# Performance work log

Hardware: AMD Instinct MI355X
Metric: run time of the kernel (lower is better)

Reference implementation:

```python
import jax, jax.numpy as jnp
import numpy as np

N, M, C = 2048, 32, 1024  # persons, max_others, dim_inner


def setup_inputs() -> dict:
    key = jax.random.key(0)
    k1, k2, k3, k4, k5, k6 = jax.random.split(key, 6)
    return {
        "person_features": jax.random.normal(k1, (N, C, 1, 1), dtype=jnp.float32),
        "other_features": jax.random.normal(k2, (N, M, C, 1, 1), dtype=jnp.float32),
        "person_boxes": jax.random.uniform(k3, (N, 4), dtype=jnp.float32),
        "other_boxes": jax.random.uniform(k4, (N, M, 4), dtype=jnp.float32),
        "is_person": jnp.ones((N, M), dtype=bool),
        "W": jax.random.normal(k5, (C, 2 * C), dtype=jnp.float32) / np.sqrt(2 * C),
        "b": jax.random.normal(k6, (C,), dtype=jnp.float32) * 0.01,
    }


def reference(person_features, other_features, person_boxes, other_boxes, is_person, W, b):
    # person_features: [n, c, 1, 1]; other_features: [n, m, c, 1, 1]
    p = person_features[:, :, 0, 0]        # [n, c]
    o = other_features[:, :, :, 0, 0]      # [n, m, c]
    # Linear on concat([p, o]) == p @ Wp^T + o @ Wo^T + b with W = [Wp | Wo]
    Wp, Wo = W[:, :p.shape[1]], W[:, p.shape[1]:]
    pk = jnp.einsum('nc,dc->nd', p, Wp)            # shared across others
    ok = jnp.einsum('nmc,dc->nmd', o, Wo)
    x = pk[:, None, :] + ok + b                    # [n, m, d]
    x = jnp.max(x, axis=1)                         # max-pool over others
    return x[:, :, None, None]                     # [n, d, 1, 1]
```

## Files before the change

### kernel.cpp

```cpp
#include <hip/hip_runtime.h>
#include <hip/hip_bf16.h>


#define NN 2048
#define MM 32
#define CC 1024

typedef __attribute__((ext_vector_type(8))) __bf16 bf16x8;
typedef __attribute__((ext_vector_type(4))) float f32x4;
typedef __attribute__((ext_vector_type(8))) unsigned short u16x8;
typedef __attribute__((ext_vector_type(4))) unsigned short u16x4;

__device__ inline unsigned short f2bf(float f) {
  union { __hip_bfloat16 h; unsigned short u; } v;
  v.h = __float2bfloat16(f);
  return v.u;
}

__device__ inline void gload_lds16(const void* g, void* l) {
  __builtin_amdgcn_global_load_lds(
      (const __attribute__((address_space(1))) void*)g,
      (__attribute__((address_space(3))) void*)l, 16, 0, 0);
}

__global__ void conv_pw(const float* __restrict__ p, const float* __restrict__ W,
                        unsigned short* __restrict__ pd,
                        unsigned short* __restrict__ wp,
                        unsigned short* __restrict__ wo) {
  const int PG = (NN * CC) / 8;
  const int WG = (CC * 2 * CC) / 8;
  int i = blockIdx.x * blockDim.x + threadIdx.x;
  int stride = gridDim.x * blockDim.x;
  for (; i < PG + WG; i += stride) {
    if (i < PG) {
      const float4* s = reinterpret_cast<const float4*>(p) + (size_t)i * 2;
      float4 a = s[0], b = s[1];
      u16x8 r;
      r[0] = f2bf(a.x); r[1] = f2bf(a.y); r[2] = f2bf(a.z); r[3] = f2bf(a.w);
      r[4] = f2bf(b.x); r[5] = f2bf(b.y); r[6] = f2bf(b.z); r[7] = f2bf(b.w);
      *reinterpret_cast<u16x8*>(pd + (size_t)i * 8) = r;
    } else {
      int f = i - PG;
      int e = f * 8;
      int d = e >> 11;
      int cc = e & 2047;
      const float4* s = reinterpret_cast<const float4*>(W) + (size_t)f * 2;
      float4 a = s[0], b = s[1];
      u16x8 r;
      r[0] = f2bf(a.x); r[1] = f2bf(a.y); r[2] = f2bf(a.z); r[3] = f2bf(a.w);
      r[4] = f2bf(b.x); r[5] = f2bf(b.y); r[6] = f2bf(b.z); r[7] = f2bf(b.w);
      unsigned short* o = (cc < CC) ? (wp + (size_t)d * CC + cc)
                                    : (wo + (size_t)d * CC + (cc - CC));
      *reinterpret_cast<u16x8*>(o) = r;
    }
  }
}

__global__ void gemm_pk(const unsigned short* __restrict__ A,
                        const unsigned short* __restrict__ B,
                        const float* __restrict__ bvec,
                        float* __restrict__ out) {
  __shared__ unsigned short As[128 * 64];
  __shared__ unsigned short Bs[128 * 64];

  int nb = gridDim.x;
  int chunk = nb >> 3;
  int obid = blockIdx.x;
  int vb = (obid & 7) * chunk + (obid >> 3);
  int bcol = vb & 7;
  int brow = vb >> 3;

  int tid = threadIdx.x;
  int l = tid & 63;
  int wid = tid >> 6;
  int wr = wid >> 1, wc = wid & 1;
  int lr = l & 15;
  int lk = (l >> 4) << 3;

  const unsigned short* gA = A + (size_t)brow * 128 * CC;
  const unsigned short* gB = B + (size_t)bcol * 128 * CC;

  f32x4 acc[4][4] = {};

  for (int kt = 0; kt < 16; ++kt) {
    int k0 = kt * 64;
#pragma unroll
    for (int j = 0; j < 4; ++j) {
      int f = (j * 256 + tid) * 8;
      int r = f >> 6;
      int c = f & 63;
      gload_lds16(gA + (size_t)r * CC + k0 + c, &As[f]);
      gload_lds16(gB + (size_t)r * CC + k0 + c, &Bs[f]);
    }
    __syncthreads();
#pragma unroll
    for (int kk = 0; kk < 2; ++kk) {
      bf16x8 af[4], bfr[4];
#pragma unroll
      for (int mi = 0; mi < 4; ++mi)
        af[mi] = *reinterpret_cast<const bf16x8*>(
            &As[(wr * 64 + mi * 16 + lr) * 64 + kk * 32 + lk]);
#pragma unroll
      for (int ni = 0; ni < 4; ++ni)
        bfr[ni] = *reinterpret_cast<const bf16x8*>(
            &Bs[(wc * 64 + ni * 16 + lr) * 64 + kk * 32 + lk]);
#pragma unroll
      for (int mi = 0; mi < 4; ++mi)
#pragma unroll
        for (int ni = 0; ni < 4; ++ni)
          acc[mi][ni] = __builtin_amdgcn_mfma_f32_16x16x32_bf16(
              af[mi], bfr[ni], acc[mi][ni], 0, 0, 0);
    }
    __syncthreads();
  }

#pragma unroll
  for (int mi = 0; mi < 4; ++mi) {
    int row = brow * 128 + wr * 64 + mi * 16 + (l >> 4) * 4;
#pragma unroll
    for (int ni = 0; ni < 4; ++ni) {
      int col = bcol * 128 + wc * 64 + ni * 16 + lr;
      float bb = bvec[col];
#pragma unroll
      for (int r = 0; r < 4; ++r)
        out[(size_t)(row + r) * CC + col] = acc[mi][ni][r] + bb;
    }
  }
}


#define BARRIER                                      \
  do {                                               \
    asm volatile("" ::: "memory");                   \
    __builtin_amdgcn_s_barrier();                    \
    asm volatile("" ::: "memory");                   \
  } while (0)

#define LGKM0 asm volatile("s_waitcnt lgkmcnt(0)" ::: "memory")
#define VMCNT(n) asm volatile("s_waitcnt vmcnt(" #n ")" ::: "memory")

#define STAGE_B(k0)                                                           \
  do {                                                                        \
    _Pragma("unroll") for (int j = 0; j < 4; ++j)                             \
        gload_lds16(gB + (size_t)(j * 64 + brr) * CC + (k0) + bsc,            \
                    lds + 16384 + ((j * 512 + tid) * 16));                    \
  } while (0)

#define ISSUE_A(k0)                                                           \
  do {                                                                        \
    _Pragma("unroll") for (int j = 0; j < 4; ++j)                             \
        aL[j] = *reinterpret_cast<const float4*>(                             \
            gAf + (size_t)(j * 32 + arow0) * CC + (k0) + ac4 * 4);            \
  } while (0)

#define CVT_WRITE_A                                                           \
  do {                                                                        \
    _Pragma("unroll") for (int j = 0; j < 4; ++j) {                           \
      u16x4 r;                                                                \
      r[0] = f2bf(aL[j].x); r[1] = f2bf(aL[j].y);                             \
      r[2] = f2bf(aL[j].z); r[3] = f2bf(aL[j].w);                             \
      *reinterpret_cast<u16x4*>(lds + (j * 32 + arow0) * 128 + aswz) = r;     \
    }                                                                         \
  } while (0)

#define MFMA16X                                                               \
  do {                                                                        \
    __builtin_amdgcn_s_setprio(1);                                            \
    _Pragma("unroll") for (int mi = 0; mi < 4; ++mi)                          \
        _Pragma("unroll") for (int ni = 0; ni < 4; ++ni)                      \
            acc[mi][ni] = __builtin_amdgcn_mfma_f32_16x16x32_bf16(            \
                af[mi], bfr[ni], acc[mi][ni], 0, 0, 0);                       \
    __builtin_amdgcn_s_setprio(0);                                            \
  } while (0)

__global__ __launch_bounds__(512, 4) void gemm_fused(
    const float* __restrict__ A,
    const unsigned short* __restrict__ B,
    const float* __restrict__ pkb,
    float* __restrict__ out) {
  __shared__ char lds[49152];

  int obid = blockIdx.x;
  int vb = (obid & 7) * 256 + (obid >> 3);
  int bcol = vb & 3;
  int brow = vb >> 2;

  int tid = threadIdx.x;
  int l = tid & 63;
  int wid = tid >> 6;
  int wr = wid >> 2;
  int wc = wid & 3;
  int lr = l & 15;
  int g = l >> 4;

  const float* gAf = A + (size_t)brow * 128 * CC;
  const unsigned short* gB = B + (size_t)bcol * 256 * CC;

  int brr = tid >> 3;
  int bsc = ((tid & 7) ^ ((tid >> 3) & 7)) * 8;

  int arow0 = tid >> 4;
  int ac4 = tid & 15;
  int aswz = (((ac4 >> 1) ^ (arow0 & 7)) * 16) + (ac4 & 1) * 8;

  int axor = lr & 7;
  int a_k0 = (wr * 64 + lr) * 128 + ((g ^ axor) * 16);
  int a_k1 = (wr * 64 + lr) * 128 + (((4 + g) ^ axor) * 16);
  int b_k0 = 16384 + (wc * 64 + lr) * 128 + ((g ^ axor) * 16);
  int b_k1 = 16384 + (wc * 64 + lr) * 128 + (((4 + g) ^ axor) * 16);

  f32x4 acc[4][4] = {};
  bf16x8 af[4], bfr[4];
  float4 aL[4];

  ISSUE_A(0);

#pragma unroll 1
  for (int t = 0; t < 16; ++t) {
    BARRIER;
    VMCNT(0);
    CVT_WRITE_A;
    STAGE_B(t * 64);
    if (t + 1 < 16) ISSUE_A((t + 1) * 64);
    LGKM0;
    if (t + 1 < 16) { VMCNT(4); } else { VMCNT(0); }
    BARRIER;
#pragma unroll
    for (int mi = 0; mi < 4; ++mi)
      af[mi] = *(const bf16x8*)(lds + a_k0 + mi * 2048);
#pragma unroll
    for (int ni = 0; ni < 4; ++ni)
      bfr[ni] = *(const bf16x8*)(lds + b_k0 + ni * 2048);
    LGKM0;
    MFMA16X;
#pragma unroll
    for (int mi = 0; mi < 4; ++mi)
      af[mi] = *(const bf16x8*)(lds + a_k1 + mi * 2048);
#pragma unroll
    for (int ni = 0; ni < 4; ++ni)
      bfr[ni] = *(const bf16x8*)(lds + b_k1 + ni * 2048);
    LGKM0;
    MFMA16X;
  }

#pragma unroll
  for (int a = 0; a < 2; ++a) {
    int n = brow * 4 + wr * 2 + a;
#pragma unroll
    for (int ni = 0; ni < 4; ++ni) {
      float v = -3.402823466e38f;
#pragma unroll
      for (int mi = 2 * a; mi < 2 * a + 2; ++mi)
#pragma unroll
        for (int r = 0; r < 4; ++r) v = fmaxf(v, acc[mi][ni][r]);
      v = fmaxf(v, __shfl_xor(v, 16));
      v = fmaxf(v, __shfl_xor(v, 32));
      if (l < 16) {
        int col = bcol * 256 + wc * 64 + ni * 16 + l;
        out[(size_t)n * CC + col] = v + pkb[(size_t)n * CC + col];
      }
    }
  }
}

extern "C" void kernel_launch(void* const* d_in, const int* in_sizes, int n_in,
                              void* d_out, int out_size, void* d_ws, size_t ws_size,
                              hipStream_t stream) {
  const float* p = (const float*)d_in[0];
  const float* o = (const float*)d_in[1];
  const float* W = (const float*)d_in[5];
  const float* b = (const float*)d_in[6];
  float* out = (float*)d_out;

  char* ws = (char*)d_ws;
  unsigned short* p_bf  = (unsigned short*)ws;
  unsigned short* wp_bf = (unsigned short*)(ws + 4194304);
  unsigned short* wo_bf = (unsigned short*)(ws + 6291456);
  float*          pkb   = (float*)(ws + 8388608);

  conv_pw<<<512, 256, 0, stream>>>(p, W, p_bf, wp_bf, wo_bf);
  gemm_pk<<<128, 256, 0, stream>>>(p_bf, wp_bf, b, pkb);
  gemm_fused<<<2048, 512, 0, stream>>>(o, wo_bf, pkb, out);
}
```

Before: 178.6 us.

## Fuse bf16 conversion and person GEMM into a single prep kernel

Folds the standalone fp32→bf16 conversion kernel and the person-feature GEMM into one launch. Blocks 0-511 convert only the Wo half of W, and the remaining 128 blocks run the pk GEMM straight from fp32 p and Wp. Those blocks convert in registers, write to swizzled LDS, and prefetch the next K-tile into registers. This removes one launch plus the bf16 round trip through memory for p and Wp. In exchange, the GEMM blocks read twice as many bytes as fp32 and do the conversion work inline.

```diff
diff --git a/kernel.cpp b/kernel.cpp
--- a/kernel.cpp
+++ b/kernel.cpp
@@ -23,50 +23,39 @@
       (__attribute__((address_space(3))) void*)l, 16, 0, 0);
 }
 
-__global__ void conv_pw(const float* __restrict__ p, const float* __restrict__ W,
-                        unsigned short* __restrict__ pd,
-                        unsigned short* __restrict__ wp,
-                        unsigned short* __restrict__ wo) {
-  const int PG = (NN * CC) / 8;
-  const int WG = (CC * 2 * CC) / 8;
-  int i = blockIdx.x * blockDim.x + threadIdx.x;
-  int stride = gridDim.x * blockDim.x;
-  for (; i < PG + WG; i += stride) {
-    if (i < PG) {
-      const float4* s = reinterpret_cast<const float4*>(p) + (size_t)i * 2;
-      float4 a = s[0], b = s[1];
-      u16x8 r;
-      r[0] = f2bf(a.x); r[1] = f2bf(a.y); r[2] = f2bf(a.z); r[3] = f2bf(a.w);
-      r[4] = f2bf(b.x); r[5] = f2bf(b.y); r[6] = f2bf(b.z); r[7] = f2bf(b.w);
-      *reinterpret_cast<u16x8*>(pd + (size_t)i * 8) = r;
-    } else {
-      int f = i - PG;
-      int e = f * 8;
-      int d = e >> 11;
-      int cc = e & 2047;
-      const float4* s = reinterpret_cast<const float4*>(W) + (size_t)f * 2;
-      float4 a = s[0], b = s[1];
-      u16x8 r;
-      r[0] = f2bf(a.x); r[1] = f2bf(a.y); r[2] = f2bf(a.z); r[3] = f2bf(a.w);
-      r[4] = f2bf(b.x); r[5] = f2bf(b.y); r[6] = f2bf(b.z); r[7] = f2bf(b.w);
-      unsigned short* o = (cc < CC) ? (wp + (size_t)d * CC + cc)
-                                    : (wo + (size_t)d * CC + (cc - CC));
-      *reinterpret_cast<u16x8*>(o) = r;
-    }
-  }
-}
-
-__global__ void gemm_pk(const unsigned short* __restrict__ A,
-                        const unsigned short* __restrict__ B,
-                        const float* __restrict__ bvec,
-                        float* __restrict__ out) {
-  __shared__ unsigned short As[128 * 64];
-  __shared__ unsigned short Bs[128 * 64];
-
-  int nb = gridDim.x;
-  int chunk = nb >> 3;
-  int obid = blockIdx.x;
-  int vb = (obid & 7) * chunk + (obid >> 3);
+#define BARRIER                                      \
+  do {                                               \
+    asm volatile("" ::: "memory");                   \
+    __builtin_amdgcn_s_barrier();                    \
+    asm volatile("" ::: "memory");                   \
+  } while (0)
+
+#define LGKM0 asm volatile("s_waitcnt lgkmcnt(0)" ::: "memory")
+#define VMCNT(n) asm volatile("s_waitcnt vmcnt(" #n ")" ::: "memory")
+
+__global__ __launch_bounds__(256, 2) void prep(
+    const float* __restrict__ p,
+    const float* __restrict__ W,
+    const float* __restrict__ bvec,
+    unsigned short* __restrict__ wo,
+    float* __restrict__ pkb) {
+  if (blockIdx.x < 512) {
+    int i = blockIdx.x * 256 + threadIdx.x;
+    int e = i * 8;
+    int d = e >> 10;
+    int c = e & 1023;
+    const float4* s = reinterpret_cast<const float4*>(W + (size_t)d * 2048 + CC + c);
+    float4 a = s[0], b = s[1];
+    u16x8 r;
+    r[0] = f2bf(a.x); r[1] = f2bf(a.y); r[2] = f2bf(a.z); r[3] = f2bf(a.w);
+    r[4] = f2bf(b.x); r[5] = f2bf(b.y); r[6] = f2bf(b.z); r[7] = f2bf(b.w);
+    *reinterpret_cast<u16x8*>(wo + (size_t)d * CC + c) = r;
+    return;
+  }
+
+  __shared__ char lds[32768];
+  int obid = blockIdx.x - 512;
+  int vb = (obid & 7) * 16 + (obid >> 3);
   int bcol = vb & 7;
   int brow = vb >> 3;
 
@@ -75,43 +64,82 @@
   int wid = tid >> 6;
   int wr = wid >> 1, wc = wid & 1;
   int lr = l & 15;
-  int lk = (l >> 4) << 3;
-
-  const unsigned short* gA = A + (size_t)brow * 128 * CC;
-  const unsigned short* gB = B + (size_t)bcol * 128 * CC;
+  int g = l >> 4;
+
+  const float* gP = p + (size_t)brow * 128 * CC;
+  const float* gW = W + (size_t)bcol * 128 * 2048;
+
+  int arow0 = tid >> 4;
+  int ac4 = tid & 15;
+  int aswz = (((ac4 >> 1) ^ (arow0 & 7)) * 16) + (ac4 & 1) * 8;
+
+  int axor = lr & 7;
+  int a_k0 = (wr * 64 + lr) * 128 + ((g ^ axor) * 16);
+  int a_k1 = (wr * 64 + lr) * 128 + (((4 + g) ^ axor) * 16);
+  int b_k0 = 16384 + (wc * 64 + lr) * 128 + ((g ^ axor) * 16);
+  int b_k1 = 16384 + (wc * 64 + lr) * 128 + (((4 + g) ^ axor) * 16);
 
   f32x4 acc[4][4] = {};
-
-  for (int kt = 0; kt < 16; ++kt) {
-    int k0 = kt * 64;
-#pragma unroll
-    for (int j = 0; j < 4; ++j) {
-      int f = (j * 256 + tid) * 8;
-      int r = f >> 6;
-      int c = f & 63;
-      gload_lds16(gA + (size_t)r * CC + k0 + c, &As[f]);
-      gload_lds16(gB + (size_t)r * CC + k0 + c, &Bs[f]);
-    }
-    __syncthreads();
-#pragma unroll
-    for (int kk = 0; kk < 2; ++kk) {
-      bf16x8 af[4], bfr[4];
-#pragma unroll
-      for (int mi = 0; mi < 4; ++mi)
-        af[mi] = *reinterpret_cast<const bf16x8*>(
-            &As[(wr * 64 + mi * 16 + lr) * 64 + kk * 32 + lk]);
-#pragma unroll
-      for (int ni = 0; ni < 4; ++ni)
-        bfr[ni] = *reinterpret_cast<const bf16x8*>(
-            &Bs[(wc * 64 + ni * 16 + lr) * 64 + kk * 32 + lk]);
-#pragma unroll
-      for (int mi = 0; mi < 4; ++mi)
-#pragma unroll
-        for (int ni = 0; ni < 4; ++ni)
-          acc[mi][ni] = __builtin_amdgcn_mfma_f32_16x16x32_bf16(
-              af[mi], bfr[ni], acc[mi][ni], 0, 0, 0);
-    }
-    __syncthreads();
+  bf16x8 af[4], bfr[4];
+  float4 aL[8], bL[8];
+
+#define ISSUE_P(k0)                                                           \
+  do {                                                                        \
+    _Pragma("unroll") for (int j = 0; j < 8; ++j)                             \
+        aL[j] = *reinterpret_cast<const float4*>(                             \
+            gP + (size_t)(j * 16 + arow0) * CC + (k0) + ac4 * 4);             \
+  } while (0)
+#define ISSUE_W(k0)                                                           \
+  do {                                                                        \
+    _Pragma("unroll") for (int j = 0; j < 8; ++j)                             \
+        bL[j] = *reinterpret_cast<const float4*>(                             \
+            gW + (size_t)(j * 16 + arow0) * 2048 + (k0) + ac4 * 4);           \
+  } while (0)
+#define CVT_WR(src, base)                                                     \
+  do {                                                                        \
+    _Pragma("unroll") for (int j = 0; j < 8; ++j) {                           \
+      u16x4 r;                                                                \
+      r[0] = f2bf(src[j].x); r[1] = f2bf(src[j].y);                           \
+      r[2] = f2bf(src[j].z); r[3] = f2bf(src[j].w);                           \
+      *reinterpret_cast<u16x4*>(lds + (base) + (j * 16 + arow0) * 128 + aswz) = r; \
+    }                                                                         \
+  } while (0)
+#define PK_MFMA                                                               \
+  do {                                                                        \
+    _Pragma("unroll") for (int mi = 0; mi < 4; ++mi)                          \
+        _Pragma("unroll") for (int ni = 0; ni < 4; ++ni)                      \
+            acc[mi][ni] = __builtin_amdgcn_mfma_f32_16x16x32_bf16(            \
+                af[mi], bfr[ni], acc[mi][ni], 0, 0, 0);                       \
+  } while (0)
+
+  ISSUE_P(0);
+  ISSUE_W(0);
+
+#pragma unroll 1
+  for (int t = 0; t < 16; ++t) {
+    BARRIER;
+    VMCNT(0);
+    CVT_WR(aL, 0);
+    CVT_WR(bL, 16384);
+    if (t + 1 < 16) { ISSUE_P((t + 1) * 64); ISSUE_W((t + 1) * 64); }
+    LGKM0;
+    BARRIER;
+#pragma unroll
+    for (int mi = 0; mi < 4; ++mi)
+      af[mi] = *(const bf16x8*)(lds + a_k0 + mi * 2048);
+#pragma unroll
+    for (int ni = 0; ni < 4; ++ni)
+      bfr[ni] = *(const bf16x8*)(lds + b_k0 + ni * 2048);
+    LGKM0;
+    PK_MFMA;
+#pragma unroll
+    for (int mi = 0; mi < 4; ++mi)
+      af[mi] = *(const bf16x8*)(lds + a_k1 + mi * 2048);
+#pragma unroll
+    for (int ni = 0; ni < 4; ++ni)
+      bfr[ni] = *(const bf16x8*)(lds + b_k1 + ni * 2048);
+    LGKM0;
+    PK_MFMA;
   }
 
 #pragma unroll
@@ -123,21 +151,15 @@
       float bb = bvec[col];
 #pragma unroll
       for (int r = 0; r < 4; ++r)
-        out[(size_t)(row + r) * CC + col] = acc[mi][ni][r] + bb;
+        pkb[(size_t)(row + r) * CC + col] = acc[mi][ni][r] + bb;
     }
   }
-}
-
-
-#define BARRIER                                      \
-  do {                                               \
-    asm volatile("" ::: "memory");                   \
-    __builtin_amdgcn_s_barrier();                    \
-    asm volatile("" ::: "memory");                   \
-  } while (0)
-
-#define LGKM0 asm volatile("s_waitcnt lgkmcnt(0)" ::: "memory")
-#define VMCNT(n) asm volatile("s_waitcnt vmcnt(" #n ")" ::: "memory")
+#undef ISSUE_P
+#undef ISSUE_W
+#undef CVT_WR
+#undef PK_MFMA
+}
+
 
 #define STAGE_B(k0)                                                           \
   do {                                                                        \
@@ -273,12 +295,9 @@
   float* out = (float*)d_out;
 
   char* ws = (char*)d_ws;
-  unsigned short* p_bf  = (unsigned short*)ws;
-  unsigned short* wp_bf = (unsigned short*)(ws + 4194304);
-  unsigned short* wo_bf = (unsigned short*)(ws + 6291456);
-  float*          pkb   = (float*)(ws + 8388608);
-
-  conv_pw<<<512, 256, 0, stream>>>(p, W, p_bf, wp_bf, wo_bf);
-  gemm_pk<<<128, 256, 0, stream>>>(p_bf, wp_bf, b, pkb);
+  unsigned short* wo_bf = (unsigned short*)ws;
+  float*          pkb   = (float*)(ws + 2097152);
+
+  prep<<<640, 256, 0, stream>>>(p, W, b, wo_bf, pkb);
   gemm_fused<<<2048, 512, 0, stream>>>(o, wo_bf, pkb, out);
 }
```

Measured after the change: 176.8 us. About the same (-1.0%).
